# Kernel optimization log

Hardware: AMD Instinct MI355X
Metric: run time of the kernel (lower is better)

Reference implementation:

```python
import jax, jax.numpy as jnp
import numpy as np


def _param(k, shape, scale=0.1):
    return (jax.random.normal(k, shape, dtype=jnp.float32) * scale)


def setup_inputs() -> dict:
    key = jax.random.key(0)
    ks = jax.random.split(key, 18)
    B, H, W = 4096, 64, 64
    inp = {
        "x": jax.random.uniform(ks[0], (B, 3, H, W), dtype=jnp.float32),
        # ImprovedColorCombinationHead: mean-RGB -> 128 -> 64 (color_semantic) -> 5 logits
        "clf_w1": _param(ks[1], (3, 128)), "clf_b1": jnp.zeros((128,), jnp.float32),
        "clf_w2": _param(ks[2], (128, 64)), "clf_b2": jnp.zeros((64,), jnp.float32),
        "clf_w3": _param(ks[3], (64, 5)), "clf_b3": jnp.zeros((5,), jnp.float32),
        # ColorRelationReasoning: 8-d one-hot color bins -> 32 (relation_features) -> 5 logits
        "rel_w1": _param(ks[4], (8, 32)), "rel_b1": jnp.zeros((32,), jnp.float32),
        "rel_w2": _param(ks[5], (32, 5)), "rel_b2": jnp.zeros((5,), jnp.float32),
        # integration_layer: Linear(10,64) ReLU Linear(64,32) ReLU Linear(32,5) (dropout=eval/identity)
        "int_w1": _param(ks[6], (10, 64)), "int_b1": jnp.zeros((64,), jnp.float32),
        "int_w2": _param(ks[7], (64, 32)), "int_b2": jnp.zeros((32,), jnp.float32),
        "int_w3": _param(ks[8], (32, 5)), "int_b3": jnp.zeros((5,), jnp.float32),
        "classifier_weight": jnp.asarray(0.7, jnp.float32),
        "reasoner_weight": jnp.asarray(0.3, jnp.float32),
    }
    return inp


def _color_bins(mean_rgb):
    # Vectorized replacement of the per-sample Python binning loop.
    r, g, b = mean_rgb[:, 0], mean_rgb[:, 1], mean_rgb[:, 2]
    conds = jnp.stack([
        (r > 0.5) & (g < 0.3) & (b < 0.3),   # red
        (r > 0.5) & (g > 0.3) & (b < 0.3),   # orange
        (r > 0.5) & (g > 0.5) & (b < 0.3),   # yellow (shadowed by prev, kept for fidelity)
        (r < 0.3) & (g > 0.5) & (b < 0.3),   # green
        (r < 0.3) & (g < 0.3) & (b > 0.5),   # blue
        (r > 0.5) & (g < 0.3) & (b > 0.5),   # magenta
        (r > 0.7) & (g > 0.7) & (b > 0.7),   # white
        (r < 0.3) & (g < 0.3) & (b < 0.3),   # black
    ], axis=0)                                # [8, B]
    any_hit = jnp.any(conds, axis=0)
    first_hit = jnp.argmax(conds, axis=0)           # first-true index = elif priority order
    fallback = jnp.argmax(mean_rgb, axis=1)         # else branch: one-hot at argmax channel (0..2)
    idx = jnp.where(any_hit, first_hit, fallback)
    return jax.nn.one_hot(idx, 8, dtype=mean_rgb.dtype)  # [B, 8]


def reference(x, clf_w1, clf_b1, clf_w2, clf_b2, clf_w3, clf_b3,
              rel_w1, rel_b1, rel_w2, rel_b2,
              int_w1, int_b1, int_w2, int_b2, int_w3, int_b3,
              classifier_weight, reasoner_weight):
    mean_rgb = jnp.mean(x, axis=(2, 3))                       # [B, 3]
    # classifier head
    h = jax.nn.relu(mean_rgb @ clf_w1 + clf_b1)
    color_semantic = jax.nn.relu(h @ clf_w2 + clf_b2)          # [B, 64]
    classifier_logits = color_semantic @ clf_w3 + clf_b3       # [B, 5]
    classifier_probs = jax.nn.softmax(classifier_logits, axis=-1)
    # relation reasoner over binned color features
    color_features = _color_bins(mean_rgb)                     # [B, 8]
    relation_features = jax.nn.relu(color_features @ rel_w1 + rel_b1)  # [B, 32]
    relation_logits = relation_features @ rel_w2 + rel_b2      # [B, 5]
    relation_probs = jax.nn.softmax(relation_logits, axis=-1)
    # integration MLP (dropout in eval mode = identity)
    combined = jnp.concatenate([classifier_probs, relation_probs], axis=-1)  # [B, 10]
    ih = jax.nn.relu(combined @ int_w1 + int_b1)
    ih = jax.nn.relu(ih @ int_w2 + int_b2)
    integrated_logits = ih @ int_w3 + int_b3
    integrated_probs = jax.nn.softmax(integrated_logits, axis=-1)
    # weighted final fusion
    final_logits = classifier_weight * classifier_logits + reasoner_weight * relation_logits
    final_probs = jax.nn.softmax(final_logits, axis=-1)
    # [B, 20]: all four prob heads concatenated
    return jnp.concatenate([classifier_probs, relation_probs, integrated_probs, final_probs], axis=-1)
```

## Files before the change

kernel.cpp:

```cpp
#include <hip/hip_runtime.h>


__device__ __forceinline__ void softmax5(const float* __restrict__ in, float* __restrict__ out) {
    float m = in[0];
#pragma unroll
    for (int i = 1; i < 5; ++i) m = fmaxf(m, in[i]);
    float e[5];
    float s = 0.f;
#pragma unroll
    for (int i = 0; i < 5; ++i) { e[i] = expf(in[i] - m); s += e[i]; }
#pragma unroll
    for (int i = 0; i < 5; ++i) out[i] = e[i] / s;
}

extern "C" __global__ void __launch_bounds__(256)
icrm_kernel(const float* __restrict__ x,
            const float* __restrict__ cw1, const float* __restrict__ cb1,
            const float* __restrict__ cw2, const float* __restrict__ cb2,
            const float* __restrict__ cw3, const float* __restrict__ cb3,
            const float* __restrict__ rw1, const float* __restrict__ rb1,
            const float* __restrict__ rw2, const float* __restrict__ rb2,
            const float* __restrict__ iw1, const float* __restrict__ ib1,
            const float* __restrict__ iw2, const float* __restrict__ ib2,
            const float* __restrict__ iw3, const float* __restrict__ ib3,
            const float* __restrict__ cwgt, const float* __restrict__ rwgt,
            float* __restrict__ out)
{
    __shared__ float  s_mean[3];
    __shared__ float  s_h[128];
    __shared__ float  s_cs[64];
    __shared__ float  s_clfl[5];
    __shared__ float  s_rell[5];
    __shared__ float  s_cf[8];
    __shared__ float  s_rf[32];
    __shared__ float  s_ih[64];
    __shared__ float  s_ih2[32];
    __shared__ float  s_intl[5];
    __shared__ float  s_finl[5];
    __shared__ float  s_outp[20];
    __shared__ double s_wsum[3][4];

    const int tid = threadIdx.x;
    const int b   = blockIdx.x;

    const float4* xb = reinterpret_cast<const float4*>(x + (size_t)b * 12288);
    double s0 = 0.0, s1 = 0.0, s2 = 0.0;
#pragma unroll
    for (int k = 0; k < 4; ++k) {
        float4 v0 = xb[tid + k * 256];
        float4 v1 = xb[1024 + tid + k * 256];
        float4 v2 = xb[2048 + tid + k * 256];
        s0 += (double)v0.x + (double)v0.y + (double)v0.z + (double)v0.w;
        s1 += (double)v1.x + (double)v1.y + (double)v1.z + (double)v1.w;
        s2 += (double)v2.x + (double)v2.y + (double)v2.z + (double)v2.w;
    }
#pragma unroll
    for (int off = 32; off > 0; off >>= 1) {
        s0 += __shfl_down(s0, off);
        s1 += __shfl_down(s1, off);
        s2 += __shfl_down(s2, off);
    }
    const int wid = tid >> 6;
    if ((tid & 63) == 0) { s_wsum[0][wid] = s0; s_wsum[1][wid] = s1; s_wsum[2][wid] = s2; }
    __syncthreads();
    if (tid < 3) {
        double t = (s_wsum[tid][0] + s_wsum[tid][1]) + (s_wsum[tid][2] + s_wsum[tid][3]);
        s_mean[tid] = (float)(t * (1.0 / 4096.0));
    }
    __syncthreads();

    if (tid < 128) {
        float a = cb1[tid]
                + s_mean[0] * cw1[tid]
                + s_mean[1] * cw1[128 + tid]
                + s_mean[2] * cw1[256 + tid];
        s_h[tid] = fmaxf(a, 0.f);
    } else if (tid == 128) {
        const float r = s_mean[0], g = s_mean[1], bl = s_mean[2];
        int idx;
        if      (r > 0.5f && g < 0.3f && bl < 0.3f) idx = 0;
        else if (r > 0.5f && g > 0.3f && bl < 0.3f) idx = 1;
        else if (r > 0.5f && g > 0.5f && bl < 0.3f) idx = 2;
        else if (r < 0.3f && g > 0.5f && bl < 0.3f) idx = 3;
        else if (r < 0.3f && g < 0.3f && bl > 0.5f) idx = 4;
        else if (r > 0.5f && g < 0.3f && bl > 0.5f) idx = 5;
        else if (r > 0.7f && g > 0.7f && bl > 0.7f) idx = 6;
        else if (r < 0.3f && g < 0.3f && bl < 0.3f) idx = 7;
        else {
            idx = 0; float m = r;
            if (g  > m) { m = g;  idx = 1; }
            if (bl > m) { m = bl; idx = 2; }
        }
#pragma unroll
        for (int j = 0; j < 8; ++j) s_cf[j] = (j == idx) ? 1.f : 0.f;
    }
    __syncthreads();

    if (tid < 64) {
        float a = cb2[tid];
        for (int k = 0; k < 128; ++k) a += s_h[k] * cw2[k * 64 + tid];
        s_cs[tid] = fmaxf(a, 0.f);
    } else if (tid >= 64 && tid < 96) {
        const int j = tid - 64;
        float a = rb1[j];
#pragma unroll
        for (int k = 0; k < 8; ++k) a += s_cf[k] * rw1[k * 32 + j];
        s_rf[j] = fmaxf(a, 0.f);
    }
    __syncthreads();

    if (tid < 5) {
        float a = cb3[tid];
        for (int k = 0; k < 64; ++k) a += s_cs[k] * cw3[k * 5 + tid];
        s_clfl[tid] = a;
    } else if (tid >= 32 && tid < 37) {
        const int j = tid - 32;
        float a = rb2[j];
        for (int k = 0; k < 32; ++k) a += s_rf[k] * rw2[k * 5 + j];
        s_rell[j] = a;
    }
    __syncthreads();

    if (tid == 0)       softmax5(s_clfl, s_outp);
    else if (tid == 64) softmax5(s_rell, s_outp + 5);
    __syncthreads();

    if (tid < 64) {
        float a = ib1[tid];
#pragma unroll
        for (int k = 0; k < 10; ++k) a += s_outp[k] * iw1[k * 64 + tid];
        s_ih[tid] = fmaxf(a, 0.f);
    }
    __syncthreads();

    if (tid < 32) {
        float a = ib2[tid];
        for (int k = 0; k < 64; ++k) a += s_ih[k] * iw2[k * 32 + tid];
        s_ih2[tid] = fmaxf(a, 0.f);
    } else if (tid >= 32 && tid < 37) {
        const int j = tid - 32;
        s_finl[j] = cwgt[0] * s_clfl[j] + rwgt[0] * s_rell[j];
    }
    __syncthreads();

    if (tid < 5) {
        float a = ib3[tid];
        for (int k = 0; k < 32; ++k) a += s_ih2[k] * iw3[k * 5 + tid];
        s_intl[tid] = a;
    }
    __syncthreads();

    if (tid == 0)       softmax5(s_intl, s_outp + 10);
    else if (tid == 64) softmax5(s_finl, s_outp + 15);
    __syncthreads();

    if (tid < 20) out[(size_t)b * 20 + tid] = s_outp[tid];
}

extern "C" void kernel_launch(void* const* d_in, const int* in_sizes, int n_in,
                              void* d_out, int out_size, void* d_ws, size_t ws_size,
                              hipStream_t stream) {
    const float* x    = (const float*)d_in[0];
    const float* cw1  = (const float*)d_in[1];
    const float* cb1  = (const float*)d_in[2];
    const float* cw2  = (const float*)d_in[3];
    const float* cb2  = (const float*)d_in[4];
    const float* cw3  = (const float*)d_in[5];
    const float* cb3  = (const float*)d_in[6];
    const float* rw1  = (const float*)d_in[7];
    const float* rb1  = (const float*)d_in[8];
    const float* rw2  = (const float*)d_in[9];
    const float* rb2  = (const float*)d_in[10];
    const float* iw1  = (const float*)d_in[11];
    const float* ib1  = (const float*)d_in[12];
    const float* iw2  = (const float*)d_in[13];
    const float* ib2  = (const float*)d_in[14];
    const float* iw3  = (const float*)d_in[15];
    const float* ib3  = (const float*)d_in[16];
    const float* cwgt = (const float*)d_in[17];
    const float* rwgt = (const float*)d_in[18];
    float* out = (float*)d_out;

    const int B = in_sizes[0] / (3 * 64 * 64);
    icrm_kernel<<<B, 256, 0, stream>>>(x, cw1, cb1, cw2, cb2, cw3, cb3,
                                       rw1, rb1, rw2, rb2,
                                       iw1, ib1, iw2, ib2, iw3, ib3,
                                       cwgt, rwgt, out);
}
```

Measured before the change: 47.89 us.

## Split fused kernel into streaming mean reduction and separate per-sample MLP kernel

Splits the single fused kernel into a bandwidth-bound mean kernel, which uses nontemporal loads and writes per-sample means to workspace, and a separate 192-thread MLP kernel that reads those means. The aim is to keep the long serial MLP tail from holding a 256-thread block, so the streaming reduction can keep more loads in flight. The cost is an extra kernel launch and a small workspace round trip. The original fused kernel is kept as a fallback when workspace is too small.

```diff
diff --git a/kernel.cpp b/kernel.cpp
--- a/kernel.cpp
+++ b/kernel.cpp
@@ -1,5 +1,7 @@
 #include <hip/hip_runtime.h>
 
+
+typedef float f4 __attribute__((ext_vector_type(4)));
 
 __device__ __forceinline__ void softmax5(const float* __restrict__ in, float* __restrict__ out) {
     float m = in[0];
@@ -14,17 +16,170 @@
 }
 
 extern "C" __global__ void __launch_bounds__(256)
-icrm_kernel(const float* __restrict__ x,
-            const float* __restrict__ cw1, const float* __restrict__ cb1,
-            const float* __restrict__ cw2, const float* __restrict__ cb2,
-            const float* __restrict__ cw3, const float* __restrict__ cb3,
-            const float* __restrict__ rw1, const float* __restrict__ rb1,
-            const float* __restrict__ rw2, const float* __restrict__ rb2,
-            const float* __restrict__ iw1, const float* __restrict__ ib1,
-            const float* __restrict__ iw2, const float* __restrict__ ib2,
-            const float* __restrict__ iw3, const float* __restrict__ ib3,
-            const float* __restrict__ cwgt, const float* __restrict__ rwgt,
-            float* __restrict__ out)
+mean_kernel(const float* __restrict__ x, float* __restrict__ means)
+{
+    __shared__ double s_wsum[3][4];
+    const int tid = threadIdx.x;
+    const int b   = blockIdx.x;
+
+    const f4* xb = reinterpret_cast<const f4*>(x + (size_t)b * 12288);
+    double s0 = 0.0, s1 = 0.0, s2 = 0.0;
+#pragma unroll
+    for (int k = 0; k < 4; ++k) {
+        f4 v0 = __builtin_nontemporal_load(xb + tid + k * 256);
+        f4 v1 = __builtin_nontemporal_load(xb + 1024 + tid + k * 256);
+        f4 v2 = __builtin_nontemporal_load(xb + 2048 + tid + k * 256);
+        s0 += (double)v0.x + (double)v0.y + (double)v0.z + (double)v0.w;
+        s1 += (double)v1.x + (double)v1.y + (double)v1.z + (double)v1.w;
+        s2 += (double)v2.x + (double)v2.y + (double)v2.z + (double)v2.w;
+    }
+#pragma unroll
+    for (int off = 32; off > 0; off >>= 1) {
+        s0 += __shfl_down(s0, off);
+        s1 += __shfl_down(s1, off);
+        s2 += __shfl_down(s2, off);
+    }
+    const int wid = tid >> 6;
+    if ((tid & 63) == 0) { s_wsum[0][wid] = s0; s_wsum[1][wid] = s1; s_wsum[2][wid] = s2; }
+    __syncthreads();
+    if (tid < 3) {
+        double t = (s_wsum[tid][0] + s_wsum[tid][1]) + (s_wsum[tid][2] + s_wsum[tid][3]);
+        means[b * 3 + tid] = (float)(t * (1.0 / 4096.0));
+    }
+}
+
+extern "C" __global__ void __launch_bounds__(192)
+mlp_kernel(const float* __restrict__ means,
+           const float* __restrict__ cw1, const float* __restrict__ cb1,
+           const float* __restrict__ cw2, const float* __restrict__ cb2,
+           const float* __restrict__ cw3, const float* __restrict__ cb3,
+           const float* __restrict__ rw1, const float* __restrict__ rb1,
+           const float* __restrict__ rw2, const float* __restrict__ rb2,
+           const float* __restrict__ iw1, const float* __restrict__ ib1,
+           const float* __restrict__ iw2, const float* __restrict__ ib2,
+           const float* __restrict__ iw3, const float* __restrict__ ib3,
+           const float* __restrict__ cwgt, const float* __restrict__ rwgt,
+           float* __restrict__ out)
+{
+    __shared__ float  s_mean[3];
+    __shared__ float  s_h[128];
+    __shared__ float  s_cs[64];
+    __shared__ float  s_clfl[5];
+    __shared__ float  s_rell[5];
+    __shared__ float  s_cf[8];
+    __shared__ float  s_rf[32];
+    __shared__ float  s_ih[64];
+    __shared__ float  s_ih2[32];
+    __shared__ float  s_intl[5];
+    __shared__ float  s_finl[5];
+    __shared__ float  s_outp[20];
+
+    const int tid = threadIdx.x;
+    const int b   = blockIdx.x;
+
+    if (tid < 3) s_mean[tid] = means[b * 3 + tid];
+    __syncthreads();
+
+    if (tid < 128) {
+        float a = cb1[tid]
+                + s_mean[0] * cw1[tid]
+                + s_mean[1] * cw1[128 + tid]
+                + s_mean[2] * cw1[256 + tid];
+        s_h[tid] = fmaxf(a, 0.f);
+    } else if (tid == 128) {
+        const float r = s_mean[0], g = s_mean[1], bl = s_mean[2];
+        int idx;
+        if      (r > 0.5f && g < 0.3f && bl < 0.3f) idx = 0;
+        else if (r > 0.5f && g > 0.3f && bl < 0.3f) idx = 1;
+        else if (r > 0.5f && g > 0.5f && bl < 0.3f) idx = 2;
+        else if (r < 0.3f && g > 0.5f && bl < 0.3f) idx = 3;
+        else if (r < 0.3f && g < 0.3f && bl > 0.5f) idx = 4;
+        else if (r > 0.5f && g < 0.3f && bl > 0.5f) idx = 5;
+        else if (r > 0.7f && g > 0.7f && bl > 0.7f) idx = 6;
+        else if (r < 0.3f && g < 0.3f && bl < 0.3f) idx = 7;
+        else {
+            idx = 0; float m = r;
+            if (g  > m) { m = g;  idx = 1; }
+            if (bl > m) { m = bl; idx = 2; }
+        }
+#pragma unroll
+        for (int j = 0; j < 8; ++j) s_cf[j] = (j == idx) ? 1.f : 0.f;
+    }
+    __syncthreads();
+
+    if (tid < 64) {
+        float a = cb2[tid];
+        for (int k = 0; k < 128; ++k) a += s_h[k] * cw2[k * 64 + tid];
+        s_cs[tid] = fmaxf(a, 0.f);
+    } else if (tid >= 64 && tid < 96) {
+        const int j = tid - 64;
+        float a = rb1[j];
+#pragma unroll
+        for (int k = 0; k < 8; ++k) a += s_cf[k] * rw1[k * 32 + j];
+        s_rf[j] = fmaxf(a, 0.f);
+    }
+    __syncthreads();
+
+    if (tid < 5) {
+        float a = cb3[tid];
+        for (int k = 0; k < 64; ++k) a += s_cs[k] * cw3[k * 5 + tid];
+        s_clfl[tid] = a;
+    } else if (tid >= 32 && tid < 37) {
+        const int j = tid - 32;
+        float a = rb2[j];
+        for (int k = 0; k < 32; ++k) a += s_rf[k] * rw2[k * 5 + j];
+        s_rell[j] = a;
+    }
+    __syncthreads();
+
+    if (tid == 0)       softmax5(s_clfl, s_outp);
+    else if (tid == 64) softmax5(s_rell, s_outp + 5);
+    __syncthreads();
+
+    if (tid < 64) {
+        float a = ib1[tid];
+#pragma unroll
+        for (int k = 0; k < 10; ++k) a += s_outp[k] * iw1[k * 64 + tid];
+        s_ih[tid] = fmaxf(a, 0.f);
+    }
+    __syncthreads();
+
+    if (tid < 32) {
+        float a = ib2[tid];
+        for (int k = 0; k < 64; ++k) a += s_ih[k] * iw2[k * 32 + tid];
+        s_ih2[tid] = fmaxf(a, 0.f);
+    } else if (tid >= 32 && tid < 37) {
+        const int j = tid - 32;
+        s_finl[j] = cwgt[0] * s_clfl[j] + rwgt[0] * s_rell[j];
+    }
+    __syncthreads();
+
+    if (tid < 5) {
+        float a = ib3[tid];
+        for (int k = 0; k < 32; ++k) a += s_ih2[k] * iw3[k * 5 + tid];
+        s_intl[tid] = a;
+    }
+    __syncthreads();
+
+    if (tid == 0)       softmax5(s_intl, s_outp + 10);
+    else if (tid == 64) softmax5(s_finl, s_outp + 15);
+    __syncthreads();
+
+    if (tid < 20) out[(size_t)b * 20 + tid] = s_outp[tid];
+}
+
+extern "C" __global__ void __launch_bounds__(256)
+icrm_fused(const float* __restrict__ x,
+           const float* __restrict__ cw1, const float* __restrict__ cb1,
+           const float* __restrict__ cw2, const float* __restrict__ cb2,
+           const float* __restrict__ cw3, const float* __restrict__ cb3,
+           const float* __restrict__ rw1, const float* __restrict__ rb1,
+           const float* __restrict__ rw2, const float* __restrict__ rb2,
+           const float* __restrict__ iw1, const float* __restrict__ ib1,
+           const float* __restrict__ iw2, const float* __restrict__ ib2,
+           const float* __restrict__ iw3, const float* __restrict__ ib3,
+           const float* __restrict__ cwgt, const float* __restrict__ rwgt,
+           float* __restrict__ out)
 {
     __shared__ float  s_mean[3];
     __shared__ float  s_h[128];
@@ -182,8 +337,18 @@
     float* out = (float*)d_out;
 
     const int B = in_sizes[0] / (3 * 64 * 64);
-    icrm_kernel<<<B, 256, 0, stream>>>(x, cw1, cb1, cw2, cb2, cw3, cb3,
-                                       rw1, rb1, rw2, rb2,
-                                       iw1, ib1, iw2, ib2, iw3, ib3,
-                                       cwgt, rwgt, out);
-}
+
+    if (ws_size >= (size_t)B * 3 * sizeof(float)) {
+        float* means = (float*)d_ws;
+        mean_kernel<<<B, 256, 0, stream>>>(x, means);
+        mlp_kernel<<<B, 192, 0, stream>>>(means, cw1, cb1, cw2, cb2, cw3, cb3,
+                                          rw1, rb1, rw2, rb2,
+                                          iw1, ib1, iw2, ib2, iw3, ib3,
+                                          cwgt, rwgt, out);
+    } else {
+        icrm_fused<<<B, 256, 0, stream>>>(x, cw1, cb1, cw2, cb2, cw3, cb3,
+                                          rw1, rb1, rw2, rb2,
+                                          iw1, ib1, iw2, ib2, iw3, ib3,
+                                          cwgt, rwgt, out);
+    }
+}
```

Measured after the change: 51.68 us. 7.9% more time.

## Stream image loads through LDS with async global_load_lds triple buffering

Applied to the files above, without the earlier changes.

Replaces the direct float4 register loads of each sample's 48KB image with per-wavefront asynchronous global-to-LDS copies into a three-slot staging buffer. Each wave owns a contiguous quarter of the image, with explicit vmcnt waits so reads of one chunk overlap the next copies. The aim is to keep more memory requests in flight and reduce register pressure in the bandwidth-bound reduction. In exchange it adds about 24KB of LDS per block, which may lower occupancy, and it relies on hand-written waitcnt ordering.

```diff
diff --git a/kernel.cpp b/kernel.cpp
--- a/kernel.cpp
+++ b/kernel.cpp
@@ -1,5 +1,19 @@
 #include <hip/hip_runtime.h>
 
+
+typedef float f4 __attribute__((ext_vector_type(4)));
+
+#define G2L(gp, lp)                                                              \
+    __builtin_amdgcn_global_load_lds(                                           \
+        (__attribute__((address_space(1))) void*)(uintptr_t)(gp),               \
+        (__attribute__((address_space(3))) void*)(uint32_t)(uintptr_t)(lp),     \
+        16, 0, 0)
+
+#define WAITVM(N)                                                \
+    do {                                                         \
+        asm volatile("s_waitcnt vmcnt(" #N ")" ::: "memory");    \
+        __builtin_amdgcn_sched_barrier(0);                       \
+    } while (0)
 
 __device__ __forceinline__ void softmax5(const float* __restrict__ in, float* __restrict__ out) {
     float m = in[0];
@@ -26,6 +40,8 @@
             const float* __restrict__ cwgt, const float* __restrict__ rwgt,
             float* __restrict__ out)
 {
+    __shared__ alignas(16) float stage[4][3][512];
+    __shared__ double s_wsum[3][4];
     __shared__ float  s_mean[3];
     __shared__ float  s_h[128];
     __shared__ float  s_cs[64];
@@ -38,30 +54,55 @@
     __shared__ float  s_intl[5];
     __shared__ float  s_finl[5];
     __shared__ float  s_outp[20];
-    __shared__ double s_wsum[3][4];
-
-    const int tid = threadIdx.x;
-    const int b   = blockIdx.x;
-
-    const float4* xb = reinterpret_cast<const float4*>(x + (size_t)b * 12288);
-    double s0 = 0.0, s1 = 0.0, s2 = 0.0;
-#pragma unroll
-    for (int k = 0; k < 4; ++k) {
-        float4 v0 = xb[tid + k * 256];
-        float4 v1 = xb[1024 + tid + k * 256];
-        float4 v2 = xb[2048 + tid + k * 256];
-        s0 += (double)v0.x + (double)v0.y + (double)v0.z + (double)v0.w;
-        s1 += (double)v1.x + (double)v1.y + (double)v1.z + (double)v1.w;
-        s2 += (double)v2.x + (double)v2.y + (double)v2.z + (double)v2.w;
-    }
+
+    const int tid  = threadIdx.x;
+    const int lane = tid & 63;
+    const int w    = tid >> 6;
+    const int b    = blockIdx.x;
+
+    const float* xg = x + (size_t)b * 12288 + 3072 * w;
+
+    double a0 = 0.0, a1 = 0.0, a2 = 0.0;
+
+#pragma unroll
+    for (int c = 0; c < 3; ++c) {
+        const float* g = xg + 512 * c;
+        float*       l = &stage[w][c][0];
+        G2L(g + lane * 4,        l);
+        G2L(g + 256 + lane * 4,  l + 256);
+    }
+
+#pragma unroll
+    for (int c = 0; c < 6; ++c) {
+        if (c < 4)        WAITVM(4);
+        else if (c == 4)  WAITVM(2);
+        else              WAITVM(0);
+
+        const int bsel = c % 3;
+        f4 u = *reinterpret_cast<const f4*>(&stage[w][bsel][lane * 4]);
+        f4 v = *reinterpret_cast<const f4*>(&stage[w][bsel][256 + lane * 4]);
+        double s = (((double)u.x + (double)u.y) + ((double)u.z + (double)u.w))
+                 + (((double)v.x + (double)v.y) + ((double)v.z + (double)v.w));
+        const int ch = (6 * w + c) >> 3;
+        if (ch == 0)      a0 += s;
+        else if (ch == 1) a1 += s;
+        else              a2 += s;
+
+        if (c + 3 < 6) {
+            const float* g = xg + 512 * (c + 3);
+            float*       l = &stage[w][bsel][0];
+            G2L(g + lane * 4,        l);
+            G2L(g + 256 + lane * 4,  l + 256);
+        }
+    }
+
 #pragma unroll
     for (int off = 32; off > 0; off >>= 1) {
-        s0 += __shfl_down(s0, off);
-        s1 += __shfl_down(s1, off);
-        s2 += __shfl_down(s2, off);
-    }
-    const int wid = tid >> 6;
-    if ((tid & 63) == 0) { s_wsum[0][wid] = s0; s_wsum[1][wid] = s1; s_wsum[2][wid] = s2; }
+        a0 += __shfl_down(a0, off);
+        a1 += __shfl_down(a1, off);
+        a2 += __shfl_down(a2, off);
+    }
+    if (lane == 0) { s_wsum[0][w] = a0; s_wsum[1][w] = a1; s_wsum[2][w] = a2; }
     __syncthreads();
     if (tid < 3) {
         double t = (s_wsum[tid][0] + s_wsum[tid][1]) + (s_wsum[tid][2] + s_wsum[tid][3]);
```

New measurement: 48.71 us. No clear change (+1.7%).
